# Performance work log

Measured on AMD Instinct MI355X. Metric: run time of the kernel, lower is better.

Reference implementation:

```python
import jax, jax.numpy as jnp
import numpy as np

B, S, K, E, H = 64, 25, 20, 256, 8
D = 2 * E  # MHA embed dim (item emb concat user emb)


def setup_inputs() -> dict:
    key = jax.random.key(0)
    ks = jax.random.split(key, 10)
    def w(k, shp, scale=0.02):
        return jax.random.normal(k, shp, jnp.float32) * scale
    return dict(
        item_embs=jax.random.normal(ks[0], (B, S, K, E), jnp.float32),
        user_embs=jax.random.normal(ks[1], (B, E), jnp.float32),
        responses=jax.random.randint(ks[2], (B, S, K), 0, 2),
        Wq=w(ks[3], (D, D)), bq=jnp.zeros((D,), jnp.float32),
        Wk=w(ks[4], (D, D)), bk=jnp.zeros((D,), jnp.float32),
        Wv=w(ks[5], (D, D)), bv=jnp.zeros((D,), jnp.float32),
        Wo=w(ks[6], (D, D)), bo=jnp.zeros((D,), jnp.float32),
        ln_g=jnp.ones((D,), jnp.float32), ln_b=jnp.zeros((D,), jnp.float32),
        W1=w(ks[7], (D, D)), b1=jnp.zeros((D,), jnp.float32),
        W2=w(ks[8], (1, D)), b2=jnp.zeros((1,), jnp.float32),
    )


def _scot_forward(item_embs, user_embs, responses, Wq, bq, Wk, bk, Wv, bv,
                  Wo, bo, ln_g, ln_b, W1, b1, W2, b2):
    Bt, St, Kt, Et = item_embs.shape
    Dt = 2 * Et
    L = St * Kt + 1  # all slate items + prepended zero item
    hd = Dt // H
    # stack_embeddings: concat item emb with broadcast user emb -> [B,S,K,2E]
    x = jnp.concatenate(
        [item_embs, jnp.broadcast_to(user_embs[:, None, None, :], (Bt, St, Kt, Et))], -1)
    x = x.reshape(Bt, St * Kt, Dt)
    # add_zero_item: prepend an all-zero token (slate number 0)
    x = jnp.concatenate([jnp.zeros((Bt, 1, Dt), x.dtype), x], axis=1)  # [B,L,D]
    # slate number per token: 0 for zero item, then 1..S repeated slate_size times
    slateno = jnp.concatenate(
        [jnp.zeros((1,), jnp.int32),
         jnp.repeat(jnp.arange(1, St + 1, dtype=jnp.int32), Kt)])  # [L]
    # clicked mask (zero item counts as clicked) -> keys visible to attention
    clicked = jnp.concatenate(
        [jnp.ones((Bt, 1), bool), responses.reshape(Bt, St * Kt) > 0], axis=1)  # [B,L]
    # attn_mask in the original blocks slateno_q <= slateno_k, except column 0;
    # combined with key_padding over non-clicked keys this equals:
    base_allow = slateno[:, None] > slateno[None, :]
    base_allow = base_allow.at[:, 0].set(True)            # zero item always visible
    allow = base_allow[None, :, :] & clicked[:, None, :]  # [B,L,L]
    # torch MultiheadAttention (batch_first)
    def heads(h):
        return h.reshape(Bt, L, H, hd).transpose(0, 2, 1, 3)  # [B,H,L,hd]
    q = heads(x @ Wq.T + bq)
    k = heads(x @ Wk.T + bk)
    v = heads(x @ Wv.T + bv)
    scores = jnp.einsum('bhqd,bhkd->bhqk', q, k) / np.sqrt(hd).astype(np.float32)
    scores = jnp.where(allow[:, None, :, :], scores, -jnp.inf)
    attn = jax.nn.softmax(scores, axis=-1)
    f = jnp.einsum('bhqk,bhkd->bhqd', attn, v)
    f = f.transpose(0, 2, 1, 3).reshape(Bt, L, Dt) @ Wo.T + bo
    f = f[:, 1:, :]  # drop zero-item query
    # out head: LayerNorm -> Linear -> GELU(exact) -> Linear
    mu = f.mean(-1, keepdims=True)
    var = ((f - mu) ** 2).mean(-1, keepdims=True)
    f = (f - mu) / jnp.sqrt(var + 1e-5) * ln_g + ln_b
    h = jax.nn.gelu(f @ W1.T + b1, approximate=False)
    out = h @ W2.T + b2  # [B, S*K, 1]
    return out.reshape(Bt, St, Kt)


def reference(item_embs, user_embs, responses, Wq, bq, Wk, bk, Wv, bv,
              Wo, bo, ln_g, ln_b, W1, b1, W2, b2):
    return _scot_forward(item_embs, user_embs, responses, Wq, bq, Wk, bk,
                         Wv, bv, Wo, bo, ln_g, ln_b, W1, b1, W2, b2)
```

## Files before the change

kernel.cpp:

```cpp
#include <hip/hip_runtime.h>
#include <math.h>

#define BATCH 64
#define SLATES 25
#define KPS 20
#define EDIM 256
#define DDIM 512
#define HEADS 8
#define HD 64
#define LFULL 501
#define NROWS 500
#define MTOT (BATCH*NROWS)
#define CMAX 512
#define NQKV 1536
#define RB 32
#define NRB ((NROWS + RB - 1) / RB)

typedef __attribute__((ext_vector_type(8))) short short8;
typedef __attribute__((ext_vector_type(4))) float f32x4;

__device__ __forceinline__ unsigned short f2bf(float x) {
    unsigned int u = __builtin_bit_cast(unsigned int, x);
    u = (u + 0x7FFFu + ((u >> 16) & 1u)) >> 16;
    return (unsigned short)u;
}
__device__ __forceinline__ float bf2f(unsigned short s) {
    unsigned int u = ((unsigned int)s) << 16;
    return __builtin_bit_cast(float, u);
}
__device__ __forceinline__ float gelu_exact(float x) {
    return 0.5f * x * (1.0f + erff(x * 0.70710678118654752440f));
}
__device__ __forceinline__ void gload16(const void* g, void* l) {
    __builtin_amdgcn_global_load_lds(
        (const __attribute__((address_space(1))) void*)g,
        (__attribute__((address_space(3))) void*)l, 16, 0, 0);
}

__global__ __launch_bounds__(256) void cvt_kernel(
    const float* __restrict__ src, unsigned short* __restrict__ dst, int n4)
{
    const int i = blockIdx.x * 256 + threadIdx.x;
    if (i >= n4) return;
    float4 v = ((const float4*)src)[i];
    ushort4 o;
    o.x = f2bf(v.x); o.y = f2bf(v.y); o.z = f2bf(v.z); o.w = f2bf(v.w);
    ((ushort4*)dst)[i] = o;
}

struct Cvt2 { const float* s[2]; unsigned short* d[2]; };
__global__ __launch_bounds__(256) void cvt2_kernel(Cvt2 a, int n4)
{
    const int i = blockIdx.x * 256 + threadIdx.x;
    if (i >= n4) return;
    const int y = blockIdx.y;
    float4 v = ((const float4*)a.s[y])[i];
    ushort4 o;
    o.x = f2bf(v.x); o.y = f2bf(v.y); o.z = f2bf(v.z); o.w = f2bf(v.w);
    ((ushort4*)a.d[y])[i] = o;
}

__global__ __launch_bounds__(256) void packqkv_kernel(
    const float* __restrict__ Wq, const float* __restrict__ Wk,
    const float* __restrict__ Wv, unsigned short* __restrict__ dst)
{
    const int y = blockIdx.y;
    const float* W = (y == 0) ? Wq : (y == 1) ? Wk : Wv;
    const int i = blockIdx.x * 256 + threadIdx.x;
    const int row = i >> 6, c4 = (i & 63) * 4;
    float4 v = *(const float4*)&W[(size_t)row * DDIM + c4];
    ushort4 o;
    o.x = f2bf(v.x); o.y = f2bf(v.y); o.z = f2bf(v.z); o.w = f2bf(v.w);
    *(ushort4*)&dst[((size_t)y * DDIM + row) * EDIM + c4] = o;
}

__global__ __launch_bounds__(64) void compact_kernel(
    const int* __restrict__ resp, int* __restrict__ cidx, int* __restrict__ cnt)
{
    const int b = blockIdx.x, lane = threadIdx.x;
    int a[8]; int c = 0;
#pragma unroll
    for (int j = 0; j < 8; ++j) {
        const int l = lane * 8 + j;
        int al = 0;
        if (l == 0) al = 1;
        else if (l <= NROWS) al = (resp[(size_t)b * NROWS + l - 1] > 0) ? 1 : 0;
        a[j] = al; c += al;
    }
    int incl = c;
#pragma unroll
    for (int off = 1; off < 64; off <<= 1) {
        int t = __shfl_up(incl, off, 64);
        if (lane >= off) incl += t;
    }
    int run = incl - c;
#pragma unroll
    for (int j = 0; j < 8; ++j) {
        const int l = lane * 8 + j;
        if (l >= 1 && l <= 481 && (l % 20) == 1)
            cnt[b * 32 + (l - 1) / 20] = run;
        cidx[b * 512 + l] = a[j] ? run : -1;
        run += a[j];
    }
}

__global__ __launch_bounds__(256) void user_bias_kernel(
    const float* __restrict__ user,
    const float* __restrict__ Wq, const float* __restrict__ bq,
    const float* __restrict__ Wk, const float* __restrict__ bk,
    const float* __restrict__ Wv, const float* __restrict__ bv,
    float* __restrict__ uball,
    unsigned short* __restrict__ qb, unsigned short* __restrict__ kc,
    unsigned short* __restrict__ vc)
{
    const int b = blockIdx.x;
    const int y = blockIdx.y;
    const int tid = threadIdx.x;
    const float* W  = (y == 0) ? Wq : (y == 1) ? Wk : Wv;
    const float* bi = (y == 0) ? bq : (y == 1) ? bk : bv;

    __shared__ float us[EDIM];
    if (tid < EDIM) us[tid] = user[b * EDIM + tid];
    __syncthreads();
    for (int o = tid; o < DDIM; o += 256) {
        float s = bi[o];
        const float* wr = &W[(size_t)o * DDIM + EDIM];
#pragma unroll 4
        for (int e = 0; e < EDIM; ++e) s += us[e] * wr[e];
        uball[(size_t)b * NQKV + y * DDIM + o] = s;
        const int hh = o >> 6, dd = o & 63;
        const size_t bh = (size_t)b * HEADS + hh;
        if (y == 0)      qb[(bh * LFULL) * HD + dd] = f2bf(bi[o]);
        else if (y == 1) kc[(bh * CMAX) * HD + dd] = f2bf(bi[o]);
        else             vc[(bh * HD + dd) * CMAX] = f2bf(bi[o]);
    }
}

__global__ __launch_bounds__(256) void gemm_qkv(
    const unsigned short* __restrict__ A,
    const unsigned short* __restrict__ Wqkv,
    const float* __restrict__ uball, const int* __restrict__ cidx,
    unsigned short* __restrict__ oq, unsigned short* __restrict__ ok,
    unsigned short* __restrict__ ov)
{
    const int tid = threadIdx.x;
    const int lin = blockIdx.y * gridDim.x + blockIdx.x;
    const int vb  = (lin & 7) * 375 + (lin >> 3);
    const int n0 = (vb % 12) * 128;
    const int m0 = (vb / 12) * 128;
    const int lane = tid & 63, wid = tid >> 6;
    const int wm = (wid & 1) * 64, wn = (wid >> 1) * 64;

    __shared__ __align__(16) unsigned short sm[24576];
    __shared__ int cids[128];
    auto As = [&](int buf) { return (unsigned short(*)[32])(sm + buf * 4096); };
    auto Ws = [&](int buf) { return (unsigned short(*)[32])(sm + 12288 + buf * 4096); };
    auto bounce = (unsigned short(*)[136])sm;

    f32x4 acc[4][4];
#pragma unroll
    for (int i = 0; i < 4; ++i)
#pragma unroll
        for (int j = 0; j < 4; ++j) acc[i][j] = (f32x4){0.f, 0.f, 0.f, 0.f};

    const unsigned short* gA0 = &A[(size_t)(m0 + wid * 16 + (lane >> 2)) * EDIM + (lane & 3) * 8];
    const unsigned short* gA1 = gA0 + (size_t)64 * EDIM;
    const unsigned short* gW0 = &Wqkv[(size_t)(n0 + wid * 16 + (lane >> 2)) * EDIM + (lane & 3) * 8];
    const unsigned short* gW1 = gW0 + (size_t)64 * EDIM;
    const int frow = lane & 15, fk = (lane >> 4) * 8;

    auto stage = [&](int buf, int k0) {
        gload16(gA0 + k0, &As(buf)[wid * 16][0]);
        gload16(gA1 + k0, &As(buf)[64 + wid * 16][0]);
        gload16(gW0 + k0, &Ws(buf)[wid * 16][0]);
        gload16(gW1 + k0, &Ws(buf)[64 + wid * 16][0]);
    };
    stage(0, 0);
    stage(1, 32);

    const int nst = EDIM / 32;
    for (int t = 0; t < nst; ++t) {
        const int cur = t % 3;
        if (t < nst - 1) asm volatile("s_waitcnt vmcnt(4)" ::: "memory");
        else             asm volatile("s_waitcnt vmcnt(0)" ::: "memory");
        __builtin_amdgcn_s_barrier();
        __builtin_amdgcn_sched_barrier(0);
        short8 af[4], wf[4];
#pragma unroll
        for (int mi = 0; mi < 4; ++mi)
            af[mi] = *(const short8*)&As(cur)[wm + mi * 16 + frow][fk];
#pragma unroll
        for (int ni = 0; ni < 4; ++ni)
            wf[ni] = *(const short8*)&Ws(cur)[wn + ni * 16 + frow][fk];
#pragma unroll
        for (int mi = 0; mi < 4; ++mi)
#pragma unroll
            for (int ni = 0; ni < 4; ++ni)
                acc[mi][ni] = __builtin_amdgcn_mfma_f32_16x16x32_bf16(
                    af[mi], wf[ni], acc[mi][ni], 0, 0, 0);
        if (t + 2 < nst) stage((t + 2) % 3, (t + 2) * 32);
    }

    const int z = n0 >> 9;
    const int b0 = m0 / NROWS;
    const int split = (b0 + 1) * NROWS;
    const int b1 = (split <= m0 + 127) ? b0 + 1 : b0;
    float ub0[4], ub1[4];
#pragma unroll
    for (int ni = 0; ni < 4; ++ni) {
        const int np = n0 + wn + ni * 16 + frow;
        ub0[ni] = uball[(size_t)b0 * NQKV + np];
        ub1[ni] = uball[(size_t)b1 * NQKV + np];
    }
    __syncthreads();
    if (z != 0 && tid < 128) {
        const int m = m0 + tid;
        const int b = (m >= split) ? b1 : b0;
        cids[tid] = cidx[b * 512 + (m - b * NROWS + 1)];
    }
#pragma unroll
    for (int mi = 0; mi < 4; ++mi)
#pragma unroll
        for (int r = 0; r < 4; ++r) {
            const int ml = wm + mi * 16 + (lane >> 4) * 4 + r;
            const bool hi = (m0 + ml >= split);
#pragma unroll
            for (int ni = 0; ni < 4; ++ni)
                bounce[ml][wn + ni * 16 + frow] =
                    f2bf(acc[mi][ni][r] + (hi ? ub1[ni] : ub0[ni]));
        }
    __syncthreads();

    const int h0 = (n0 & 511) >> 6;
    if (z == 0) {
        const int row = tid >> 1, half = tid & 1;
        const int m = m0 + row;
        const int b = (m >= split) ? b1 : b0;
        const int l = m - b * NROWS + 1;
        unsigned short* dst = &oq[(((size_t)b * HEADS + h0 + half) * LFULL + l) * HD];
        const unsigned short* src = &bounce[row][half * 64];
#pragma unroll
        for (int j = 0; j < 8; ++j)
            *(uint4*)(dst + j * 8) = *(const uint4*)(src + j * 8);
    } else if (z == 1) {
        const int row = tid >> 1, half = tid & 1;
        const int c = cids[row];
        if (c >= 0) {
            const int m = m0 + row;
            const int b = (m >= split) ? b1 : b0;
            unsigned short* dst = &ok[(((size_t)b * HEADS + h0 + half) * CMAX + c) * HD];
            const unsigned short* src = &bounce[row][half * 64];
#pragma unroll
            for (int j = 0; j < 8; ++j)
                *(uint4*)(dst + j * 8) = *(const uint4*)(src + j * 8);
        }
    } else {
        const int col = tid & 127, mh = tid >> 7;
        const int hh = h0 + (col >> 6), dd = col & 63;
        for (int mm = 0; mm < 64; ++mm) {
            const int row = mh * 64 + mm;
            const int c = cids[row];
            if (c >= 0) {
                const int m = m0 + row;
                const int b = (m >= split) ? b1 : b0;
                ov[((size_t)b * HEADS + hh) * (size_t)(HD * CMAX)
                   + (size_t)dd * CMAX + c] = bounce[row][col];
            }
        }
    }
}

template <int MODE>
__global__ __launch_bounds__(256) void gemm_bf16(
    const unsigned short* __restrict__ A,
    const unsigned short* __restrict__ W,
    const float* __restrict__ bias, void* __restrict__ outp,
    const float* __restrict__ W2, float* __restrict__ part)
{
    const int tid = threadIdx.x;
    const int lin = blockIdx.y * gridDim.x + blockIdx.x;
    const int vb  = (lin & 7) * 125 + (lin >> 3);
    const int n0 = (vb % 4) * 128;
    const int m0 = (vb / 4) * 128;
    const int lane = tid & 63, wid = tid >> 6;
    const int wm = (wid & 1) * 64, wn = (wid >> 1) * 64;

    __shared__ unsigned short As[3][128][32];
    __shared__ unsigned short Ws[3][128][32];

    f32x4 acc[4][4];
#pragma unroll
    for (int i = 0; i < 4; ++i)
#pragma unroll
        for (int j = 0; j < 4; ++j) acc[i][j] = (f32x4){0.f, 0.f, 0.f, 0.f};

    const unsigned short* gA0 = &A[(size_t)(m0 + wid * 16 + (lane >> 2)) * DDIM + (lane & 3) * 8];
    const unsigned short* gA1 = gA0 + (size_t)64 * DDIM;
    const unsigned short* gW0 = &W[(size_t)(n0 + wid * 16 + (lane >> 2)) * DDIM + (lane & 3) * 8];
    const unsigned short* gW1 = gW0 + (size_t)64 * DDIM;
    const int frow = lane & 15, fk = (lane >> 4) * 8;

    auto stage = [&](int buf, int k0) {
        gload16(gA0 + k0, &As[buf][wid * 16][0]);
        gload16(gA1 + k0, &As[buf][64 + wid * 16][0]);
        gload16(gW0 + k0, &Ws[buf][wid * 16][0]);
        gload16(gW1 + k0, &Ws[buf][64 + wid * 16][0]);
    };
    stage(0, 0);
    stage(1, 32);

    const int nst = DDIM / 32;
    for (int t = 0; t < nst; ++t) {
        const int cur = t % 3;
        if (t < nst - 1) asm volatile("s_waitcnt vmcnt(4)" ::: "memory");
        else             asm volatile("s_waitcnt vmcnt(0)" ::: "memory");
        __builtin_amdgcn_s_barrier();
        __builtin_amdgcn_sched_barrier(0);
        short8 af[4], wf[4];
#pragma unroll
        for (int mi = 0; mi < 4; ++mi)
            af[mi] = *(const short8*)&As[cur][wm + mi * 16 + frow][fk];
#pragma unroll
        for (int ni = 0; ni < 4; ++ni)
            wf[ni] = *(const short8*)&Ws[cur][wn + ni * 16 + frow][fk];
#pragma unroll
        for (int mi = 0; mi < 4; ++mi)
#pragma unroll
            for (int ni = 0; ni < 4; ++ni)
                acc[mi][ni] = __builtin_amdgcn_mfma_f32_16x16x32_bf16(
                    af[mi], wf[ni], acc[mi][ni], 0, 0, 0);
        if (t + 2 < nst) stage((t + 2) % 3, (t + 2) * 32);
    }

    if (MODE == 1) {
#pragma unroll
        for (int mi = 0; mi < 4; ++mi)
#pragma unroll
            for (int ni = 0; ni < 4; ++ni) {
                const int n = n0 + wn + ni * 16 + frow;
                const float bv = bias[n];
#pragma unroll
                for (int r = 0; r < 4; ++r) {
                    const int m = m0 + wm + mi * 16 + (lane >> 4) * 4 + r;
                    ((unsigned short*)outp)[(size_t)m * DDIM + n] =
                        f2bf(acc[mi][ni][r] + bv);
                }
            }
    } else {
        float w2v[4], bv4[4];
#pragma unroll
        for (int ni = 0; ni < 4; ++ni) {
            const int n = n0 + wn + ni * 16 + frow;
            w2v[ni] = W2[n];
            bv4[ni] = bias[n];
        }
        float ps[4][4];
#pragma unroll
        for (int mi = 0; mi < 4; ++mi)
#pragma unroll
            for (int r = 0; r < 4; ++r) ps[mi][r] = 0.f;
#pragma unroll
        for (int mi = 0; mi < 4; ++mi)
#pragma unroll
            for (int ni = 0; ni < 4; ++ni)
#pragma unroll
                for (int r = 0; r < 4; ++r)
                    ps[mi][r] += gelu_exact(acc[mi][ni][r] + bv4[ni]) * w2v[ni];
        const int slot = (n0 >> 7) * 2 + (wn >> 6);
#pragma unroll
        for (int mi = 0; mi < 4; ++mi)
#pragma unroll
            for (int r = 0; r < 4; ++r) {
                float s = ps[mi][r];
                s += __shfl_xor(s, 1, 64);
                s += __shfl_xor(s, 2, 64);
                s += __shfl_xor(s, 4, 64);
                s += __shfl_xor(s, 8, 64);
                if (frow == 0) {
                    const int m = m0 + wm + mi * 16 + (lane >> 4) * 4 + r;
                    part[(size_t)m * 8 + slot] = s;
                }
            }
    }
}

__global__ __launch_bounds__(256) void w2red_kernel(
    const float* __restrict__ part, const float* __restrict__ b2,
    float* __restrict__ out)
{
    const int m = blockIdx.x * 256 + threadIdx.x;
    if (m >= MTOT) return;
    const float* p = part + (size_t)m * 8;
    float s = b2[0];
#pragma unroll
    for (int i = 0; i < 8; ++i) s += p[i];
    out[m] = s;
}

__global__ __launch_bounds__(256) void attn_mfma(
    const unsigned short* __restrict__ qx, const unsigned short* __restrict__ kc,
    const unsigned short* __restrict__ vc, const int* __restrict__ cnt,
    unsigned short* __restrict__ outb)
{
    const int lin = blockIdx.x + NRB * (blockIdx.y + HEADS * blockIdx.z);
    const int vbk = (lin & 7) * (NRB * HEADS * BATCH / 8) + (lin >> 3);
    const int rbk = vbk % NRB;
    const int h   = (vbk / NRB) % HEADS;
    const int b   = vbk / (NRB * HEADS);
    const int g0  = rbk * RB;

    const int tid = threadIdx.x, lane = tid & 63, w = tid >> 6;

    __shared__ __align__(16) unsigned short scb[RB][520];
    __shared__ float rsw[4][RB];
    __shared__ int snck[RB];

    const int frow = lane & 15, fk = (lane >> 4) * 8;
    const size_t bh = (size_t)b * HEADS + h;
    const unsigned short* kbase = kc + bh * (CMAX * HD);
    const unsigned short* vbase = vc + bh * (HD * CMAX);

    if (tid < RB) {
        const int s = (g0 + tid >= NROWS ? NROWS - 1 : g0 + tid) / KPS;
        snck[tid] = cnt[b * 32 + s];
    }

    short8 qf[2][2];
#pragma unroll
    for (int mi = 0; mi < 2; ++mi) {
        const int qrow = g0 + mi * 16 + frow;
#pragma unroll
        for (int ks = 0; ks < 2; ++ks) {
            short8 v = {};
            if (qrow < NROWS)
                v = *(const short8*)&qx[(bh * LFULL + qrow + 1) * HD + ks * 32 + fk];
            qf[mi][ks] = v;
        }
    }
    __syncthreads();

    int nck8[2][4];
#pragma unroll
    for (int mi = 0; mi < 2; ++mi)
#pragma unroll
        for (int r = 0; r < 4; ++r)
            nck8[mi][r] = snck[mi * 16 + (lane >> 4) * 4 + r];
    const int nmax = snck[RB - 1];
    const int NT = (nmax + 63) >> 6;

    f32x4 rsum[2];
    rsum[0] = (f32x4){0.f, 0.f, 0.f, 0.f};
    rsum[1] = (f32x4){0.f, 0.f, 0.f, 0.f};
    for (int t = 0; t < NT; ++t) {
        const int key = (t << 6) + w * 16 + frow;
        const unsigned short* kr = kbase + (size_t)key * HD;
        const short8 kf0 = *(const short8*)(kr + fk);
        const short8 kf1 = *(const short8*)(kr + 32 + fk);
        f32x4 s2[2];
#pragma unroll
        for (int mi = 0; mi < 2; ++mi) {
            s2[mi] = (f32x4){0.f, 0.f, 0.f, 0.f};
            s2[mi] = __builtin_amdgcn_mfma_f32_16x16x32_bf16(qf[mi][0], kf0, s2[mi], 0, 0, 0);
            s2[mi] = __builtin_amdgcn_mfma_f32_16x16x32_bf16(qf[mi][1], kf1, s2[mi], 0, 0, 0);
        }
#pragma unroll
        for (int mi = 0; mi < 2; ++mi)
#pragma unroll
            for (int r = 0; r < 4; ++r) {
                const int row = mi * 16 + (lane >> 4) * 4 + r;
                const float p = (key < nck8[mi][r]) ? __expf(s2[mi][r] * 0.125f) : 0.f;
                rsum[mi][r] += p;
                scb[row][key] = f2bf(p);
            }
    }
#pragma unroll
    for (int mi = 0; mi < 2; ++mi)
#pragma unroll
        for (int r = 0; r < 4; ++r) {
            float v = rsum[mi][r];
            v += __shfl_xor(v, 1, 64);
            v += __shfl_xor(v, 2, 64);
            v += __shfl_xor(v, 4, 64);
            v += __shfl_xor(v, 8, 64);
            if (frow == 0)
                rsw[w][mi * 16 + (lane >> 4) * 4 + r] = v;
        }
    __syncthreads();

    f32x4 po[2];
    po[0] = (f32x4){0.f, 0.f, 0.f, 0.f};
    po[1] = (f32x4){0.f, 0.f, 0.f, 0.f};
    const unsigned short* vrow = vbase + (size_t)(w * 16 + frow) * CMAX;
    for (int t = 0; t < NT; ++t) {
#pragma unroll
        for (int ks = 0; ks < 2; ++ks) {
            const int kb0 = (t << 6) + ks * 32 + fk;
            const short8 vf = *(const short8*)(vrow + kb0);
#pragma unroll
            for (int mi = 0; mi < 2; ++mi) {
                const short8 pf = *(const short8*)&scb[mi * 16 + frow][kb0];
                po[mi] = __builtin_amdgcn_mfma_f32_16x16x32_bf16(pf, vf, po[mi], 0, 0, 0);
            }
        }
    }

#pragma unroll
    for (int mi = 0; mi < 2; ++mi)
#pragma unroll
        for (int r = 0; r < 4; ++r) {
            const int row = mi * 16 + (lane >> 4) * 4 + r;
            const int m = g0 + row;
            if (m < NROWS) {
                const float inv = 1.0f / (rsw[0][row] + rsw[1][row]
                                        + rsw[2][row] + rsw[3][row]);
                outb[((size_t)b * NROWS + m) * DDIM
                     + h * HD + w * 16 + frow] = f2bf(po[mi][r] * inv);
            }
        }
}

__global__ __launch_bounds__(256) void ln_kernel(
    const unsigned short* __restrict__ f, const float* __restrict__ g,
    const float* __restrict__ bt, unsigned short* __restrict__ o)
{
    const int row = blockIdx.x * 4 + (threadIdx.x >> 6);
    const int lane = threadIdx.x & 63;
    const size_t base = (size_t)row * DDIM + lane * 8;
    short8 v = *(const short8*)&f[base];
    float xv[8];
    float s = 0.f;
#pragma unroll
    for (int i = 0; i < 8; ++i) { xv[i] = bf2f((unsigned short)v[i]); s += xv[i]; }
#pragma unroll
    for (int off = 32; off; off >>= 1) s += __shfl_xor(s, off, 64);
    const float mu = s * (1.0f / DDIM);
    float var = 0.f;
#pragma unroll
    for (int i = 0; i < 8; ++i) { const float d0 = xv[i] - mu; var += d0 * d0; }
#pragma unroll
    for (int off = 32; off; off >>= 1) var += __shfl_xor(var, off, 64);
    const float rs = rsqrtf(var * (1.0f / DDIM) + 1e-5f);
    short8 ov;
#pragma unroll
    for (int i = 0; i < 8; ++i) {
        const int d0 = lane * 8 + i;
        ov[i] = (short)f2bf((xv[i] - mu) * rs * g[d0] + bt[d0]);
    }
    *(short8*)&o[base] = ov;
}

extern "C" void kernel_launch(void* const* d_in, const int* in_sizes, int n_in,
                              void* d_out, int out_size, void* d_ws, size_t ws_size,
                              hipStream_t stream)
{
    const float* item = (const float*)d_in[0];
    const float* user = (const float*)d_in[1];
    const int*   resp = (const int*)d_in[2];
    const float* Wq = (const float*)d_in[3];  const float* bq = (const float*)d_in[4];
    const float* Wk = (const float*)d_in[5];  const float* bk = (const float*)d_in[6];
    const float* Wv = (const float*)d_in[7];  const float* bv = (const float*)d_in[8];
    const float* Wo = (const float*)d_in[9];  const float* bo = (const float*)d_in[10];
    const float* lng = (const float*)d_in[11]; const float* lnb = (const float*)d_in[12];
    const float* W1 = (const float*)d_in[13]; const float* b1 = (const float*)d_in[14];
    const float* W2 = (const float*)d_in[15]; const float* b2 = (const float*)d_in[16];
    float* out = (float*)d_out;

    char* p = (char*)d_ws;
    auto alloc = [&](size_t bytes) { char* r = p; p += (bytes + 255) & ~(size_t)255; return r; };
    const size_t NITEM = (size_t)BATCH * NROWS * EDIM;
    const size_t NW    = (size_t)DDIM * DDIM;
    const size_t NQ    = (size_t)BATCH * HEADS * LFULL * HD;
    const size_t NC    = (size_t)BATCH * HEADS * CMAX * HD;
    const size_t NMD   = (size_t)MTOT * DDIM;
    const size_t PAD   = 8192;

    unsigned short* itemb  = (unsigned short*)alloc(NITEM * 2);
    unsigned short* Wqkvb  = (unsigned short*)alloc((size_t)NQKV * EDIM * 2);
    unsigned short* Wob    = (unsigned short*)alloc(NW * 2);
    unsigned short* W1b    = (unsigned short*)alloc(NW * 2);
    unsigned short* qb     = (unsigned short*)alloc(NQ * 2 + PAD);
    unsigned short* kcb    = (unsigned short*)alloc(NC * 2 + PAD);
    unsigned short* vcb    = (unsigned short*)alloc(NC * 2 + PAD);
    unsigned short* aob    = (unsigned short*)alloc(NMD * 2);
    unsigned short* fb16   = (unsigned short*)alloc(NMD * 2);
    float* uball = (float*)alloc((size_t)BATCH * NQKV * 4);
    float* part  = (float*)alloc((size_t)MTOT * 8 * 4);
    int* cidx    = (int*)alloc((size_t)BATCH * 512 * 4);
    int* cnt     = (int*)alloc((size_t)BATCH * 32 * 4);

    cvt_kernel<<<dim3((NITEM / 4 + 255) / 256), 256, 0, stream>>>(item, itemb, NITEM / 4);
    packqkv_kernel<<<dim3(DDIM * EDIM / 4 / 256, 3), 256, 0, stream>>>(Wq, Wk, Wv, Wqkvb);
    Cvt2 c2;
    c2.s[0] = Wo; c2.s[1] = W1; c2.d[0] = Wob; c2.d[1] = W1b;
    cvt2_kernel<<<dim3(NW / 4 / 256, 2), 256, 0, stream>>>(c2, NW / 4);

    compact_kernel<<<dim3(BATCH), 64, 0, stream>>>(resp, cidx, cnt);

    user_bias_kernel<<<dim3(BATCH, 3), 256, 0, stream>>>(
        user, Wq, bq, Wk, bk, Wv, bv, uball, qb, kcb, vcb);

    gemm_qkv<<<dim3(NQKV / 128, MTOT / 128), 256, 0, stream>>>(
        itemb, Wqkvb, uball, cidx, qb, kcb, vcb);

    attn_mfma<<<dim3(NRB, HEADS, BATCH), 256, 0, stream>>>(qb, kcb, vcb, cnt, aob);

    dim3 gg(DDIM / 128, MTOT / 128);
    gemm_bf16<1><<<gg, 256, 0, stream>>>(aob, Wob, bo, fb16, nullptr, nullptr);
    ln_kernel<<<dim3(MTOT / 4), 256, 0, stream>>>(fb16, lng, lnb, aob);
    gemm_bf16<2><<<gg, 256, 0, stream>>>(aob, W1b, b1, nullptr, W2, part);
    w2red_kernel<<<dim3((MTOT + 255) / 256), 256, 0, stream>>>(part, b2, out);
}
```

Baseline: 280.7 us.

## Fold LayerNorm into W1 GEMM using row stats from Wo GEMM epilogue

Removes the standalone LayerNorm pass. The Wo GEMM epilogue now emits per-row partial sums and sums of squares, and a tiny kernel turns them into mean and rstd. Gamma is folded into a prescaled bf16 W1, and the W1·beta and W1·gamma row sums are precomputed, so the W1 GEMM reads the un-normalized activations and applies the normalization algebraically in its epilogue. This saves a full read and write of the activation matrix. In exchange it uses a single-pass E[x²]−mu² variance and applies the normalization after the bf16 matmul, which may change numerical accuracy.

```diff
diff --git a/kernel.cpp b/kernel.cpp
--- a/kernel.cpp
+++ b/kernel.cpp
@@ -48,18 +48,6 @@
     ((ushort4*)dst)[i] = o;
 }
 
-struct Cvt2 { const float* s[2]; unsigned short* d[2]; };
-__global__ __launch_bounds__(256) void cvt2_kernel(Cvt2 a, int n4)
-{
-    const int i = blockIdx.x * 256 + threadIdx.x;
-    if (i >= n4) return;
-    const int y = blockIdx.y;
-    float4 v = ((const float4*)a.s[y])[i];
-    ushort4 o;
-    o.x = f2bf(v.x); o.y = f2bf(v.y); o.z = f2bf(v.z); o.w = f2bf(v.w);
-    ((ushort4*)a.d[y])[i] = o;
-}
-
 __global__ __launch_bounds__(256) void packqkv_kernel(
     const float* __restrict__ Wq, const float* __restrict__ Wk,
     const float* __restrict__ Wv, unsigned short* __restrict__ dst)
@@ -72,6 +60,31 @@
     ushort4 o;
     o.x = f2bf(v.x); o.y = f2bf(v.y); o.z = f2bf(v.z); o.w = f2bf(v.w);
     *(ushort4*)&dst[((size_t)y * DDIM + row) * EDIM + c4] = o;
+}
+
+__global__ __launch_bounds__(256) void w1prep_kernel(
+    const float* __restrict__ W1, const float* __restrict__ g,
+    const float* __restrict__ lnb, unsigned short* __restrict__ W1g,
+    float2* __restrict__ c1c2)
+{
+    const int row = blockIdx.x * 4 + (threadIdx.x >> 6);
+    const int lane = threadIdx.x & 63;
+    float c1 = 0.f, c2 = 0.f;
+#pragma unroll
+    for (int i = 0; i < 8; ++i) {
+        const int k = lane + i * 64;
+        const float w = W1[(size_t)row * DDIM + k];
+        const float gv = g[k];
+        c1 += w * lnb[k];
+        c2 += w * gv;
+        W1g[(size_t)row * DDIM + k] = f2bf(w * gv);
+    }
+#pragma unroll
+    for (int off = 32; off; off >>= 1) {
+        c1 += __shfl_xor(c1, off, 64);
+        c2 += __shfl_xor(c2, off, 64);
+    }
+    if (lane == 0) c1c2[row] = make_float2(c1, c2);
 }
 
 __global__ __launch_bounds__(64) void compact_kernel(
@@ -275,7 +288,8 @@
     const unsigned short* __restrict__ A,
     const unsigned short* __restrict__ W,
     const float* __restrict__ bias, void* __restrict__ outp,
-    const float* __restrict__ W2, float* __restrict__ part)
+    const float* __restrict__ W2, float* __restrict__ part,
+    const float2* __restrict__ musr, const float2* __restrict__ c1c2)
 {
     const int tid = threadIdx.x;
     const int lin = blockIdx.y * gridDim.x + blockIdx.x;
@@ -332,56 +346,76 @@
         if (t + 2 < nst) stage((t + 2) % 3, (t + 2) * 32);
     }
 
+    const int slot = (n0 >> 7) * 2 + (wn >> 6);
     if (MODE == 1) {
+        float bv4[4];
+#pragma unroll
+        for (int ni = 0; ni < 4; ++ni) bv4[ni] = bias[n0 + wn + ni * 16 + frow];
 #pragma unroll
         for (int mi = 0; mi < 4; ++mi)
 #pragma unroll
-            for (int ni = 0; ni < 4; ++ni) {
-                const int n = n0 + wn + ni * 16 + frow;
-                const float bv = bias[n];
-#pragma unroll
-                for (int r = 0; r < 4; ++r) {
-                    const int m = m0 + wm + mi * 16 + (lane >> 4) * 4 + r;
-                    ((unsigned short*)outp)[(size_t)m * DDIM + n] =
-                        f2bf(acc[mi][ni][r] + bv);
+            for (int r = 0; r < 4; ++r) {
+                const int m = m0 + wm + mi * 16 + (lane >> 4) * 4 + r;
+                float s1 = 0.f, s2 = 0.f;
+#pragma unroll
+                for (int ni = 0; ni < 4; ++ni) {
+                    const float v = acc[mi][ni][r] + bv4[ni];
+                    s1 += v; s2 += v * v;
+                    ((unsigned short*)outp)[(size_t)m * DDIM + n0 + wn + ni * 16 + frow]
+                        = f2bf(v);
+                }
+                s1 += __shfl_xor(s1, 1, 64); s2 += __shfl_xor(s2, 1, 64);
+                s1 += __shfl_xor(s1, 2, 64); s2 += __shfl_xor(s2, 2, 64);
+                s1 += __shfl_xor(s1, 4, 64); s2 += __shfl_xor(s2, 4, 64);
+                s1 += __shfl_xor(s1, 8, 64); s2 += __shfl_xor(s2, 8, 64);
+                if (frow == 0) {
+                    part[((size_t)m << 4) + slot * 2]     = s1;
+                    part[((size_t)m << 4) + slot * 2 + 1] = s2;
                 }
             }
     } else {
-        float w2v[4], bv4[4];
+        float w2v[4], cb[4], c2v[4];
 #pragma unroll
         for (int ni = 0; ni < 4; ++ni) {
             const int n = n0 + wn + ni * 16 + frow;
             w2v[ni] = W2[n];
-            bv4[ni] = bias[n];
-        }
-        float ps[4][4];
+            const float2 cc = c1c2[n];
+            cb[ni]  = cc.x + bias[n];
+            c2v[ni] = cc.y;
+        }
 #pragma unroll
         for (int mi = 0; mi < 4; ++mi)
 #pragma unroll
-            for (int r = 0; r < 4; ++r) ps[mi][r] = 0.f;
-#pragma unroll
-        for (int mi = 0; mi < 4; ++mi)
-#pragma unroll
-            for (int ni = 0; ni < 4; ++ni)
-#pragma unroll
-                for (int r = 0; r < 4; ++r)
-                    ps[mi][r] += gelu_exact(acc[mi][ni][r] + bv4[ni]) * w2v[ni];
-        const int slot = (n0 >> 7) * 2 + (wn >> 6);
-#pragma unroll
-        for (int mi = 0; mi < 4; ++mi)
-#pragma unroll
             for (int r = 0; r < 4; ++r) {
-                float s = ps[mi][r];
+                const int m = m0 + wm + mi * 16 + (lane >> 4) * 4 + r;
+                const float2 ms = musr[m];
+                float s = 0.f;
+#pragma unroll
+                for (int ni = 0; ni < 4; ++ni)
+                    s += gelu_exact(ms.y * (acc[mi][ni][r] - ms.x * c2v[ni]) + cb[ni])
+                         * w2v[ni];
                 s += __shfl_xor(s, 1, 64);
                 s += __shfl_xor(s, 2, 64);
                 s += __shfl_xor(s, 4, 64);
                 s += __shfl_xor(s, 8, 64);
-                if (frow == 0) {
-                    const int m = m0 + wm + mi * 16 + (lane >> 4) * 4 + r;
+                if (frow == 0)
                     part[(size_t)m * 8 + slot] = s;
-                }
             }
     }
+}
+
+__global__ __launch_bounds__(256) void lnstats_kernel(
+    const float* __restrict__ rowpart, float2* __restrict__ musr)
+{
+    const int m = blockIdx.x * 256 + threadIdx.x;
+    if (m >= MTOT) return;
+    const float* p = rowpart + ((size_t)m << 4);
+    float s1 = 0.f, s2 = 0.f;
+#pragma unroll
+    for (int i = 0; i < 8; ++i) { s1 += p[i * 2]; s2 += p[i * 2 + 1]; }
+    const float mu = s1 * (1.0f / DDIM);
+    const float var = s2 * (1.0f / DDIM) - mu * mu;
+    musr[m] = make_float2(mu, rsqrtf(var + 1e-5f));
 }
 
 __global__ __launch_bounds__(256) void w2red_kernel(
@@ -517,36 +551,6 @@
                      + h * HD + w * 16 + frow] = f2bf(po[mi][r] * inv);
             }
         }
-}
-
-__global__ __launch_bounds__(256) void ln_kernel(
-    const unsigned short* __restrict__ f, const float* __restrict__ g,
-    const float* __restrict__ bt, unsigned short* __restrict__ o)
-{
-    const int row = blockIdx.x * 4 + (threadIdx.x >> 6);
-    const int lane = threadIdx.x & 63;
-    const size_t base = (size_t)row * DDIM + lane * 8;
-    short8 v = *(const short8*)&f[base];
-    float xv[8];
-    float s = 0.f;
-#pragma unroll
-    for (int i = 0; i < 8; ++i) { xv[i] = bf2f((unsigned short)v[i]); s += xv[i]; }
-#pragma unroll
-    for (int off = 32; off; off >>= 1) s += __shfl_xor(s, off, 64);
-    const float mu = s * (1.0f / DDIM);
-    float var = 0.f;
-#pragma unroll
-    for (int i = 0; i < 8; ++i) { const float d0 = xv[i] - mu; var += d0 * d0; }
-#pragma unroll
-    for (int off = 32; off; off >>= 1) var += __shfl_xor(var, off, 64);
-    const float rs = rsqrtf(var * (1.0f / DDIM) + 1e-5f);
-    short8 ov;
-#pragma unroll
-    for (int i = 0; i < 8; ++i) {
-        const int d0 = lane * 8 + i;
-        ov[i] = (short)f2bf((xv[i] - mu) * rs * g[d0] + bt[d0]);
-    }
-    *(short8*)&o[base] = ov;
 }
 
 extern "C" void kernel_launch(void* const* d_in, const int* in_sizes, int n_in,
@@ -577,22 +581,24 @@
     unsigned short* itemb  = (unsigned short*)alloc(NITEM * 2);
     unsigned short* Wqkvb  = (unsigned short*)alloc((size_t)NQKV * EDIM * 2);
     unsigned short* Wob    = (unsigned short*)alloc(NW * 2);
-    unsigned short* W1b    = (unsigned short*)alloc(NW * 2);
+    unsigned short* W1gb   = (unsigned short*)alloc(NW * 2);
     unsigned short* qb     = (unsigned short*)alloc(NQ * 2 + PAD);
     unsigned short* kcb    = (unsigned short*)alloc(NC * 2 + PAD);
     unsigned short* vcb    = (unsigned short*)alloc(NC * 2 + PAD);
     unsigned short* aob    = (unsigned short*)alloc(NMD * 2);
     unsigned short* fb16   = (unsigned short*)alloc(NMD * 2);
-    float* uball = (float*)alloc((size_t)BATCH * NQKV * 4);
-    float* part  = (float*)alloc((size_t)MTOT * 8 * 4);
+    float*  uball  = (float*)alloc((size_t)BATCH * NQKV * 4);
+    float*  part   = (float*)alloc((size_t)MTOT * 8 * 4);
+    float*  rowpart= (float*)alloc((size_t)MTOT * 16 * 4);
+    float2* musr   = (float2*)alloc((size_t)MTOT * 8);
+    float2* c1c2   = (float2*)alloc((size_t)DDIM * 8);
     int* cidx    = (int*)alloc((size_t)BATCH * 512 * 4);
     int* cnt     = (int*)alloc((size_t)BATCH * 32 * 4);
 
     cvt_kernel<<<dim3((NITEM / 4 + 255) / 256), 256, 0, stream>>>(item, itemb, NITEM / 4);
     packqkv_kernel<<<dim3(DDIM * EDIM / 4 / 256, 3), 256, 0, stream>>>(Wq, Wk, Wv, Wqkvb);
-    Cvt2 c2;
-    c2.s[0] = Wo; c2.s[1] = W1; c2.d[0] = Wob; c2.d[1] = W1b;
-    cvt2_kernel<<<dim3(NW / 4 / 256, 2), 256, 0, stream>>>(c2, NW / 4);
+    cvt_kernel<<<dim3(NW / 4 / 256), 256, 0, stream>>>(Wo, Wob, NW / 4);
+    w1prep_kernel<<<dim3(DDIM / 4), 256, 0, stream>>>(W1, lng, lnb, W1gb, c1c2);
 
     compact_kernel<<<dim3(BATCH), 64, 0, stream>>>(resp, cidx, cnt);
 
@@ -605,8 +611,10 @@
     attn_mfma<<<dim3(NRB, HEADS, BATCH), 256, 0, stream>>>(qb, kcb, vcb, cnt, aob);
 
     dim3 gg(DDIM / 128, MTOT / 128);
-    gemm_bf16<1><<<gg, 256, 0, stream>>>(aob, Wob, bo, fb16, nullptr, nullptr);
-    ln_kernel<<<dim3(MTOT / 4), 256, 0, stream>>>(fb16, lng, lnb, aob);
-    gemm_bf16<2><<<gg, 256, 0, stream>>>(aob, W1b, b1, nullptr, W2, part);
+    gemm_bf16<1><<<gg, 256, 0, stream>>>(aob, Wob, bo, fb16, nullptr, rowpart,
+                                         nullptr, nullptr);
+    lnstats_kernel<<<dim3((MTOT + 255) / 256), 256, 0, stream>>>(rowpart, musr);
+    gemm_bf16<2><<<gg, 256, 0, stream>>>(fb16, W1gb, b1, nullptr, W2, part,
+                                         musr, c1c2);
     w2red_kernel<<<dim3((MTOT + 255) / 256), 256, 0, stream>>>(part, b2, out);
 }
```

Measured after the change: 257.5 us. 1.09x faster.
